# Kernel optimization log

Measured on AMD Instinct MI355X. Metric: run time of the kernel, lower is better.

Reference implementation:

```python
import jax, jax.numpy as jnp
import numpy as np

EPS = 1e-12  # matches torch F.normalize default


def _l2norm_c(x):
    # normalize along channel dim (axis=1) of [B,C,H,W]
    n = jnp.sqrt(jnp.sum(x * x, axis=1, keepdims=True))
    return x / jnp.maximum(n, EPS)


def setup_inputs() -> dict:
    key = jax.random.key(0)
    ks = jax.random.split(key, 6)
    B, C, H, W = 2, 256, 64, 64
    return {
        "sv": jax.random.normal(ks[0], (B, 1, H, W), dtype=jnp.float32),
        "si": jax.random.normal(ks[1], (B, 1, H, W), dtype=jnp.float32),
        "sf": jax.random.normal(ks[2], (B, 1, H, W), dtype=jnp.float32),
        "dv": jax.random.normal(ks[3], (B, C, H, W), dtype=jnp.float32),
        "di": jax.random.normal(ks[4], (B, C, H, W), dtype=jnp.float32),
        "df": jax.random.normal(ks[5], (B, C, H, W), dtype=jnp.float32),
    }


def reference(sv, si, sf, dv, di, df):
    # keypoint score loss: L1(sf, max(sv, si))
    kp = jnp.mean(jnp.abs(sf - jnp.maximum(sv, si)))
    # descriptor loss: L1(df, (dv+di)/2)
    desc = jnp.mean(jnp.abs(df - (dv + di) * 0.5))
    # match loss (dense): normalize along C, full correlation volumes, L1
    a = _l2norm_c(dv)
    b = _l2norm_c(di)
    c = _l2norm_c(df)
    sim_ab = jnp.einsum('bchw,bcij->bhwij', a, b)  # [B,H,W,H,W]
    sim_ac = jnp.einsum('bchw,bcij->bhwij', a, c)
    match = jnp.mean(jnp.abs(sim_ac - sim_ab))
    return kp + desc + match
```

## Files before the change

### kernel.cpp

```cpp
#include <hip/hip_runtime.h>
#include <hip/hip_bf16.h>
#include <math.h>

#define BB 2
#define CC 256
#define CCP (CC + 2)
#define HWN 4096
#define PT 32
#define TM 128

typedef __attribute__((ext_vector_type(4))) int   intx4;
typedef __attribute__((ext_vector_type(8))) int   intx8;
typedef __attribute__((ext_vector_type(4))) float floatx4;

__device__ __forceinline__ unsigned short f2bf(float f) {
    union { float f; unsigned u; } v; v.f = f;
    unsigned r = v.u + 0x7FFF + ((v.u >> 16) & 1);
    return (unsigned short)(r >> 16);
}

__device__ __forceinline__ float bf2f(unsigned short h) {
    union { unsigned u; float f; } v; v.u = ((unsigned)h) << 16;
    return v.f;
}

__device__ __forceinline__ void load_lds16(const void* g, void* l) {
    __builtin_amdgcn_global_load_lds(
        (const __attribute__((address_space(1))) unsigned int*)g,
        (__attribute__((address_space(3))) unsigned int*)l, 16, 0, 0);
}

__global__ __launch_bounds__(1024) void prep_kernel(
    const float* __restrict__ sv, const float* __restrict__ si,
    const float* __restrict__ sf, const float* __restrict__ dv,
    const float* __restrict__ di, const float* __restrict__ df,
    unsigned char* __restrict__ Af8, unsigned char* __restrict__ Df8,
    float* __restrict__ pk, float* __restrict__ pd)
{
    __shared__ unsigned short lv[PT][CCP];
    __shared__ unsigned short li[PT][CCP];
    __shared__ unsigned short lf[PT][CCP];
    __shared__ float ssq[3][PT];
    __shared__ float inv[3][PT];
    __shared__ float sdesc;

    const int b   = blockIdx.x / (HWN / PT);
    const int p0  = (blockIdx.x % (HWN / PT)) * PT;
    const int tid = threadIdx.x;
    const int tp  = tid & (PT - 1);
    const int cs  = tid >> 5;

    if (tid < 3 * PT) ((float*)ssq)[tid] = 0.0f;
    if (tid == 0) sdesc = 0.0f;
    __syncthreads();

    float sqv = 0.f, sqi = 0.f, sqf = 0.f, descp = 0.f;
    const size_t base = (size_t)b * CC * HWN + p0 + tp;
    #pragma unroll
    for (int j = 0; j < 8; ++j) {
        const int c = cs * 8 + j;
        const size_t idx = base + (size_t)c * HWN;
        const float v = dv[idx], ii = di[idx], ff = df[idx];
        descp += fabsf(ff - 0.5f * (v + ii));
        sqv += v * v; sqi += ii * ii; sqf += ff * ff;
        lv[tp][c] = f2bf(v); li[tp][c] = f2bf(ii); lf[tp][c] = f2bf(ff);
    }
    sqv += __shfl_down(sqv, 32);
    sqi += __shfl_down(sqi, 32);
    sqf += __shfl_down(sqf, 32);
    if ((tid & 63) < 32) {
        atomicAdd(&ssq[0][tp], sqv);
        atomicAdd(&ssq[1][tp], sqi);
        atomicAdd(&ssq[2][tp], sqf);
    }

    #pragma unroll
    for (int off = 32; off > 0; off >>= 1) descp += __shfl_down(descp, off);
    if ((tid & 63) == 0) atomicAdd(&sdesc, descp);

    if (tid < 64) {
        float kpv = 0.f;
        if (tid < PT) {
            const size_t sidx = (size_t)b * HWN + p0 + tid;
            kpv = fabsf(sf[sidx] - fmaxf(sv[sidx], si[sidx]));
        }
        #pragma unroll
        for (int off = 32; off > 0; off >>= 1) kpv += __shfl_down(kpv, off);
        if (tid == 0) pk[blockIdx.x] = kpv;
    }
    __syncthreads();

    if (tid < 3 * PT) {
        const float s = ((float*)ssq)[tid];
        ((float*)inv)[tid] = 1.0f / fmaxf(sqrtf(s), 1e-12f);
    }
    __syncthreads();

    if (tid == 0) pd[blockIdx.x] = sdesc;

    int* Ao = (int*)(Af8 + ((size_t)b * HWN + p0) * CC);
    int* Do = (int*)(Df8 + ((size_t)b * HWN + p0) * CC);
    #pragma unroll
    for (int i = tid; i < PT * CC / 4; i += 1024) {
        const int p = i >> 6, c0 = (i & 63) * 4;
        const float ia = inv[0][p], ib = inv[1][p], ic = inv[2][p];
        float a0 = bf2f(lv[p][c0 + 0]) * ia, a1 = bf2f(lv[p][c0 + 1]) * ia;
        float a2 = bf2f(lv[p][c0 + 2]) * ia, a3 = bf2f(lv[p][c0 + 3]) * ia;
        float d0 = bf2f(lf[p][c0 + 0]) * ic - bf2f(li[p][c0 + 0]) * ib;
        float d1 = bf2f(lf[p][c0 + 1]) * ic - bf2f(li[p][c0 + 1]) * ib;
        float d2 = bf2f(lf[p][c0 + 2]) * ic - bf2f(li[p][c0 + 2]) * ib;
        float d3 = bf2f(lf[p][c0 + 3]) * ic - bf2f(li[p][c0 + 3]) * ib;
        int wa = __builtin_amdgcn_cvt_pk_fp8_f32(a0, a1, 0, false);
        wa     = __builtin_amdgcn_cvt_pk_fp8_f32(a2, a3, wa, true);
        int wd = __builtin_amdgcn_cvt_pk_fp8_f32(d0, d1, 0, false);
        wd     = __builtin_amdgcn_cvt_pk_fp8_f32(d2, d3, wd, true);
        Ao[i] = wa;
        Do[i] = wd;
    }
}

__global__ __launch_bounds__(256) void gemm_abs_kernel(
    const unsigned char* __restrict__ Af8,
    const unsigned char* __restrict__ Df8,
    float* __restrict__ pg)
{
    __shared__ unsigned char lA[TM * CC];
    __shared__ unsigned char lB[TM * CC];

    const int b    = blockIdx.z;
    const int bm   = blockIdx.x * TM;
    const int bn   = blockIdx.y * TM;
    const int tid  = threadIdx.x;
    const int wave = tid >> 6;
    const int lane = tid & 63;
    const int wr   = wave >> 1, wc = wave & 1;

    const unsigned char* Agb = Af8 + (size_t)b * HWN * CC + (size_t)bm * CC;
    const unsigned char* Dgb = Df8 + (size_t)b * HWN * CC + (size_t)bn * CC;

    #pragma unroll
    for (int i = 0; i < 8; ++i) {
        const int r0 = wave * 32 + i * 4;
        const int r  = r0 + (lane >> 4);
        const int cs = (lane & 15) ^ (r & 15);
        const size_t gof = (size_t)r * CC + cs * 16;
        load_lds16(Agb + gof, (char*)lA + r0 * CC);
        load_lds16(Dgb + gof, (char*)lB + r0 * CC);
    }
    __syncthreads();

    floatx4 accf[4][4];
    #pragma unroll
    for (int mi = 0; mi < 4; ++mi)
        #pragma unroll
        for (int ni = 0; ni < 4; ++ni)
            accf[mi][ni] = (floatx4){0.f, 0.f, 0.f, 0.f};

    #pragma unroll
    for (int ks = 0; ks < 2; ++ks) {
        const int cb = ks * 8 + (lane >> 4) * 2;
        intx8 a8[4], b8[4];
        #pragma unroll
        for (int mi = 0; mi < 4; ++mi) {
            const int m = wr * 64 + mi * 16 + (lane & 15);
            const char* pa = (const char*)lA + m * CC;
            intx4 lo = *(const intx4*)(pa + ((cb    ) ^ (m & 15)) * 16);
            intx4 hi = *(const intx4*)(pa + ((cb + 1) ^ (m & 15)) * 16);
            a8[mi] = __builtin_shufflevector(lo, hi, 0, 1, 2, 3, 4, 5, 6, 7);
        }
        #pragma unroll
        for (int ni = 0; ni < 4; ++ni) {
            const int n = wc * 64 + ni * 16 + (lane & 15);
            const char* pb = (const char*)lB + n * CC;
            intx4 lo = *(const intx4*)(pb + ((cb    ) ^ (n & 15)) * 16);
            intx4 hi = *(const intx4*)(pb + ((cb + 1) ^ (n & 15)) * 16);
            b8[ni] = __builtin_shufflevector(lo, hi, 0, 1, 2, 3, 4, 5, 6, 7);
        }
        #pragma unroll
        for (int mi = 0; mi < 4; ++mi)
            #pragma unroll
            for (int ni = 0; ni < 4; ++ni)
                accf[mi][ni] = __builtin_amdgcn_mfma_scale_f32_16x16x128_f8f6f4(
                    a8[mi], b8[ni], accf[mi][ni],
                    0, 0,
                    0, 0x7F7F7F7F,
                    0, 0x7F7F7F7F);
    }

    float s = 0.f;
    #pragma unroll
    for (int mi = 0; mi < 4; ++mi)
        #pragma unroll
        for (int ni = 0; ni < 4; ++ni)
            #pragma unroll
            for (int r = 0; r < 4; ++r)
                s += fabsf(accf[mi][ni][r]);
    #pragma unroll
    for (int off = 32; off > 0; off >>= 1) s += __shfl_down(s, off);
    if (lane == 0) {
        const int flat = blockIdx.x + 32 * (blockIdx.y + 32 * blockIdx.z);
        pg[flat * 4 + wave] = s;
    }
}

__global__ __launch_bounds__(256) void final_kernel(
    const float* __restrict__ pg, const float* __restrict__ pk,
    const float* __restrict__ pd, float* __restrict__ out)
{
    __shared__ float ws[4];
    const int t = threadIdx.x;
    float s = 0.f;
    #pragma unroll
    for (int i = 0; i < 32; ++i)
        s += pg[t + i * 256];
    s *= (1.0f / 33554432.0f);
    s += pk[t] * (1.0f / 8192.0f)
       + pd[t] * (1.0f / 2097152.0f);
    #pragma unroll
    for (int off = 32; off > 0; off >>= 1) s += __shfl_down(s, off);
    if ((t & 63) == 0) ws[t >> 6] = s;
    __syncthreads();
    if (t == 0) out[0] = ws[0] + ws[1] + ws[2] + ws[3];
}

extern "C" void kernel_launch(void* const* d_in, const int* in_sizes, int n_in,
                              void* d_out, int out_size, void* d_ws, size_t ws_size,
                              hipStream_t stream) {
    const float* sv = (const float*)d_in[0];
    const float* si = (const float*)d_in[1];
    const float* sf = (const float*)d_in[2];
    const float* dv = (const float*)d_in[3];
    const float* di = (const float*)d_in[4];
    const float* df = (const float*)d_in[5];

    unsigned char* Af8 = (unsigned char*)d_ws;
    unsigned char* Df8 = Af8 + (size_t)BB * HWN * CC;
    float* pg = (float*)(Df8 + (size_t)BB * HWN * CC);
    float* pk = pg + 8192;
    float* pd = pk + 256;

    prep_kernel<<<dim3(BB * (HWN / PT)), 1024, 0, stream>>>(
        sv, si, sf, dv, di, df, Af8, Df8, pk, pd);
    gemm_abs_kernel<<<dim3(HWN / TM, HWN / TM, BB), 256, 0, stream>>>(
        Af8, Df8, pg);
    final_kernel<<<1, 256, 0, stream>>>(pg, pk, pd, (float*)d_out);
}
```

Before: 95.79 us.

## Vectorize prep loads and fuse final reduction into GEMM via last-block counter

The prep kernel now has each thread load float4 vectors covering four pixels and two channels, replacing strided scalar loads. Per-pixel squared sums are reduced with wider shuffles before the shared atomics. The final reduction kernel is removed: each GEMM block writes one partial sum, and the last block to finish, found through a global atomic counter, does the final sum. This removes one kernel launch and reduces partial-sum traffic, at the cost of a threadfence plus an atomic per block and a serial tail in the last block.

```diff
diff --git a/kernel.cpp b/kernel.cpp
--- a/kernel.cpp
+++ b/kernel.cpp
@@ -8,6 +8,7 @@
 #define HWN 4096
 #define PT 32
 #define TM 128
+#define NBLK (32 * 32 * BB)
 
 typedef __attribute__((ext_vector_type(4))) int   intx4;
 typedef __attribute__((ext_vector_type(8))) int   intx8;
@@ -35,7 +36,8 @@
     const float* __restrict__ sf, const float* __restrict__ dv,
     const float* __restrict__ di, const float* __restrict__ df,
     unsigned char* __restrict__ Af8, unsigned char* __restrict__ Df8,
-    float* __restrict__ pk, float* __restrict__ pd)
+    float* __restrict__ pk, float* __restrict__ pd,
+    unsigned int* __restrict__ cnt)
 {
     __shared__ unsigned short lv[PT][CCP];
     __shared__ unsigned short li[PT][CCP];
@@ -47,31 +49,54 @@
     const int b   = blockIdx.x / (HWN / PT);
     const int p0  = (blockIdx.x % (HWN / PT)) * PT;
     const int tid = threadIdx.x;
-    const int tp  = tid & (PT - 1);
-    const int cs  = tid >> 5;
+    const int tp4 = tid & 7;
+    const int c0  = (tid >> 3) * 2;
 
     if (tid < 3 * PT) ((float*)ssq)[tid] = 0.0f;
-    if (tid == 0) sdesc = 0.0f;
-    __syncthreads();
-
-    float sqv = 0.f, sqi = 0.f, sqf = 0.f, descp = 0.f;
-    const size_t base = (size_t)b * CC * HWN + p0 + tp;
-    #pragma unroll
-    for (int j = 0; j < 8; ++j) {
-        const int c = cs * 8 + j;
-        const size_t idx = base + (size_t)c * HWN;
-        const float v = dv[idx], ii = di[idx], ff = df[idx];
-        descp += fabsf(ff - 0.5f * (v + ii));
-        sqv += v * v; sqi += ii * ii; sqf += ff * ff;
-        lv[tp][c] = f2bf(v); li[tp][c] = f2bf(ii); lf[tp][c] = f2bf(ff);
-    }
-    sqv += __shfl_down(sqv, 32);
-    sqi += __shfl_down(sqi, 32);
-    sqf += __shfl_down(sqf, 32);
-    if ((tid & 63) < 32) {
-        atomicAdd(&ssq[0][tp], sqv);
-        atomicAdd(&ssq[1][tp], sqi);
-        atomicAdd(&ssq[2][tp], sqf);
+    if (tid == 0) {
+        sdesc = 0.0f;
+        if (blockIdx.x == 0) *cnt = 0u;
+    }
+    __syncthreads();
+
+    const size_t rbase = ((size_t)b * CC + c0) * HWN + p0 + tp4 * 4;
+    const floatx4 v0 = *(const floatx4*)(dv + rbase);
+    const floatx4 v1 = *(const floatx4*)(dv + rbase + HWN);
+    const floatx4 i0 = *(const floatx4*)(di + rbase);
+    const floatx4 i1 = *(const floatx4*)(di + rbase + HWN);
+    const floatx4 f0 = *(const floatx4*)(df + rbase);
+    const floatx4 f1 = *(const floatx4*)(df + rbase + HWN);
+
+    float sqv[4], sqi[4], sqf[4], descp = 0.f;
+    #pragma unroll
+    for (int k = 0; k < 4; ++k) {
+        sqv[k] = v0[k] * v0[k] + v1[k] * v1[k];
+        sqi[k] = i0[k] * i0[k] + i1[k] * i1[k];
+        sqf[k] = f0[k] * f0[k] + f1[k] * f1[k];
+        descp += fabsf(f0[k] - 0.5f * (v0[k] + i0[k]))
+               + fabsf(f1[k] - 0.5f * (v1[k] + i1[k]));
+        const int p = tp4 * 4 + k;
+        *(unsigned*)&lv[p][c0] = (unsigned)f2bf(v0[k]) | ((unsigned)f2bf(v1[k]) << 16);
+        *(unsigned*)&li[p][c0] = (unsigned)f2bf(i0[k]) | ((unsigned)f2bf(i1[k]) << 16);
+        *(unsigned*)&lf[p][c0] = (unsigned)f2bf(f0[k]) | ((unsigned)f2bf(f1[k]) << 16);
+    }
+
+    #pragma unroll
+    for (int off = 8; off < 64; off <<= 1) {
+        #pragma unroll
+        for (int k = 0; k < 4; ++k) {
+            sqv[k] += __shfl_down(sqv[k], off);
+            sqi[k] += __shfl_down(sqi[k], off);
+            sqf[k] += __shfl_down(sqf[k], off);
+        }
+    }
+    if ((tid & 63) < 8) {
+        #pragma unroll
+        for (int k = 0; k < 4; ++k) {
+            atomicAdd(&ssq[0][tp4 * 4 + k], sqv[k]);
+            atomicAdd(&ssq[1][tp4 * 4 + k], sqi[k]);
+            atomicAdd(&ssq[2][tp4 * 4 + k], sqf[k]);
+        }
     }
 
     #pragma unroll
@@ -102,14 +127,14 @@
     int* Do = (int*)(Df8 + ((size_t)b * HWN + p0) * CC);
     #pragma unroll
     for (int i = tid; i < PT * CC / 4; i += 1024) {
-        const int p = i >> 6, c0 = (i & 63) * 4;
+        const int p = i >> 6, cc0 = (i & 63) * 4;
         const float ia = inv[0][p], ib = inv[1][p], ic = inv[2][p];
-        float a0 = bf2f(lv[p][c0 + 0]) * ia, a1 = bf2f(lv[p][c0 + 1]) * ia;
-        float a2 = bf2f(lv[p][c0 + 2]) * ia, a3 = bf2f(lv[p][c0 + 3]) * ia;
-        float d0 = bf2f(lf[p][c0 + 0]) * ic - bf2f(li[p][c0 + 0]) * ib;
-        float d1 = bf2f(lf[p][c0 + 1]) * ic - bf2f(li[p][c0 + 1]) * ib;
-        float d2 = bf2f(lf[p][c0 + 2]) * ic - bf2f(li[p][c0 + 2]) * ib;
-        float d3 = bf2f(lf[p][c0 + 3]) * ic - bf2f(li[p][c0 + 3]) * ib;
+        float a0 = bf2f(lv[p][cc0 + 0]) * ia, a1 = bf2f(lv[p][cc0 + 1]) * ia;
+        float a2 = bf2f(lv[p][cc0 + 2]) * ia, a3 = bf2f(lv[p][cc0 + 3]) * ia;
+        float d0 = bf2f(lf[p][cc0 + 0]) * ic - bf2f(li[p][cc0 + 0]) * ib;
+        float d1 = bf2f(lf[p][cc0 + 1]) * ic - bf2f(li[p][cc0 + 1]) * ib;
+        float d2 = bf2f(lf[p][cc0 + 2]) * ic - bf2f(li[p][cc0 + 2]) * ib;
+        float d3 = bf2f(lf[p][cc0 + 3]) * ic - bf2f(li[p][cc0 + 3]) * ib;
         int wa = __builtin_amdgcn_cvt_pk_fp8_f32(a0, a1, 0, false);
         wa     = __builtin_amdgcn_cvt_pk_fp8_f32(a2, a3, wa, true);
         int wd = __builtin_amdgcn_cvt_pk_fp8_f32(d0, d1, 0, false);
@@ -122,10 +147,14 @@
 __global__ __launch_bounds__(256) void gemm_abs_kernel(
     const unsigned char* __restrict__ Af8,
     const unsigned char* __restrict__ Df8,
-    float* __restrict__ pg)
+    float* __restrict__ pg, const float* __restrict__ pk,
+    const float* __restrict__ pd, unsigned int* __restrict__ cnt,
+    float* __restrict__ out)
 {
     __shared__ unsigned char lA[TM * CC];
     __shared__ unsigned char lB[TM * CC];
+    __shared__ float wsum[4];
+    __shared__ int lastflag;
 
     const int b    = blockIdx.z;
     const int bm   = blockIdx.x * TM;
@@ -197,30 +226,33 @@
                 s += fabsf(accf[mi][ni][r]);
     #pragma unroll
     for (int off = 32; off > 0; off >>= 1) s += __shfl_down(s, off);
-    if (lane == 0) {
-        const int flat = blockIdx.x + 32 * (blockIdx.y + 32 * blockIdx.z);
-        pg[flat * 4 + wave] = s;
-    }
-}
-
-__global__ __launch_bounds__(256) void final_kernel(
-    const float* __restrict__ pg, const float* __restrict__ pk,
-    const float* __restrict__ pd, float* __restrict__ out)
-{
-    __shared__ float ws[4];
-    const int t = threadIdx.x;
-    float s = 0.f;
-    #pragma unroll
-    for (int i = 0; i < 32; ++i)
-        s += pg[t + i * 256];
-    s *= (1.0f / 33554432.0f);
-    s += pk[t] * (1.0f / 8192.0f)
-       + pd[t] * (1.0f / 2097152.0f);
-    #pragma unroll
-    for (int off = 32; off > 0; off >>= 1) s += __shfl_down(s, off);
-    if ((t & 63) == 0) ws[t >> 6] = s;
-    __syncthreads();
-    if (t == 0) out[0] = ws[0] + ws[1] + ws[2] + ws[3];
+    if (lane == 0) wsum[wave] = s;
+    __syncthreads();
+
+    const int flat = blockIdx.x + 32 * (blockIdx.y + 32 * blockIdx.z);
+    if (tid == 0) {
+        pg[flat] = wsum[0] + wsum[1] + wsum[2] + wsum[3];
+        __threadfence();
+        const unsigned old = atomicAdd(cnt, 1u);
+        lastflag = (old == NBLK - 1) ? 1 : 0;
+    }
+    __syncthreads();
+
+    if (lastflag) {
+        __threadfence();
+        float r = 0.f;
+        #pragma unroll
+        for (int i = 0; i < NBLK / 256; ++i)
+            r += pg[tid + i * 256];
+        r *= (1.0f / 33554432.0f);
+        r += pk[tid] * (1.0f / 8192.0f)
+           + pd[tid] * (1.0f / 2097152.0f);
+        #pragma unroll
+        for (int off = 32; off > 0; off >>= 1) r += __shfl_down(r, off);
+        if (lane == 0) wsum[wave] = r;
+        __syncthreads();
+        if (tid == 0) out[0] = wsum[0] + wsum[1] + wsum[2] + wsum[3];
+    }
 }
 
 extern "C" void kernel_launch(void* const* d_in, const int* in_sizes, int n_in,
@@ -236,12 +268,12 @@
     unsigned char* Af8 = (unsigned char*)d_ws;
     unsigned char* Df8 = Af8 + (size_t)BB * HWN * CC;
     float* pg = (float*)(Df8 + (size_t)BB * HWN * CC);
-    float* pk = pg + 8192;
+    float* pk = pg + NBLK;
     float* pd = pk + 256;
+    unsigned int* cnt = (unsigned int*)(pd + 256);
 
     prep_kernel<<<dim3(BB * (HWN / PT)), 1024, 0, stream>>>(
-        sv, si, sf, dv, di, df, Af8, Df8, pk, pd);
+        sv, si, sf, dv, di, df, Af8, Df8, pk, pd, cnt);
     gemm_abs_kernel<<<dim3(HWN / TM, HWN / TM, BB), 256, 0, stream>>>(
-        Af8, Df8, pg);
-    final_kernel<<<1, 256, 0, stream>>>(pg, pk, pd, (float*)d_out);
-}
+        Af8, Df8, pg, pk, pd, cnt, (float*)d_out);
+}
```

Measured after the change: 139.0 us. 1.45x slower.
